# Kernel optimization log

Hardware: AMD Instinct MI355X
Metric: run time of the kernel (lower is better)

Reference implementation:

```python
import jax, jax.numpy as jnp
import numpy as np

B, DIM, H, W = 8, 384, 64, 64
HEADS, KD, RATIO = 8, 32, 2
D = RATIO * KD            # 64, per-head value dim
NH_KD = HEADS * KD        # 256
DH = HEADS * D            # 512
N = H * W


def conv1x1_bn(x, Wc, scale, bias):
    # 1x1 conv (no bias) + BatchNorm2d in eval mode folds to per-channel affine.
    y = jnp.einsum('bchw,oc->bohw', x, Wc)
    return y * scale[:, None, None] + bias[:, None, None]


def setup_inputs() -> dict:
    key = jax.random.key(0)
    ks = jax.random.split(key, 13)
    f32 = jnp.float32
    inp = {
        'x': jax.random.normal(ks[0], (B, DIM, H, W), f32),
        'Wq': jax.random.normal(ks[1], (NH_KD, DIM), f32) * (1.0 / np.sqrt(DIM)),
        'sq': jax.random.uniform(ks[2], (NH_KD,), f32, 0.5, 1.5),
        'bq': jax.random.normal(ks[3], (NH_KD,), f32) * 0.1,
        'Wk': jax.random.normal(ks[4], (NH_KD, DIM), f32) * (1.0 / np.sqrt(DIM)),
        'sk': jax.random.uniform(ks[5], (NH_KD,), f32, 0.5, 1.5),
        'bk': jax.random.normal(ks[6], (NH_KD,), f32) * 0.1,
        'Wv': jax.random.normal(ks[7], (DH, DIM), f32) * (1.0 / np.sqrt(DIM)),
        'sv': jax.random.uniform(ks[8], (DH,), f32, 0.5, 1.5),
        'bv': jax.random.normal(ks[9], (DH,), f32) * 0.1,
        'Wp': jax.random.normal(ks[10], (DIM, DH), f32) * (1.0 / np.sqrt(DH)),
        'sp': jax.random.uniform(ks[11], (DIM,), f32, 0.5, 1.5),
        'bp': jax.random.normal(ks[12], (DIM,), f32) * 0.1,
    }
    return inp


def reference(x, Wq, sq, bq, Wk, sk, bk, Wv, sv, bv, Wp, sp, bp):
    # Q/K/V projections (1x1 conv + BN), reshaped to per-head [B, h, c, N]
    q = conv1x1_bn(x, Wq, sq, bq).reshape(B, HEADS, KD, N)
    k = conv1x1_bn(x, Wk, sk, bk).reshape(B, HEADS, KD, N)
    v = conv1x1_bn(x, Wv, sv, bv).reshape(B, HEADS, D, N)
    # dual softmax: keys over spatial dim, queries over channel dim
    key_sm = jax.nn.softmax(k, axis=3)
    query_sm = jax.nn.softmax(q, axis=2)
    # context = key @ value^T : [B,h,kd,d]
    context = jnp.einsum('bhkn,bhdn->bhkd', key_sm, v)
    # attended = context^T @ query : [B,h,d,N]
    attended = jnp.einsum('bhkd,bhkn->bhdn', context, query_sm)
    attended = attended.reshape(B, DH, H, W)
    # proj: activation (ReLU) then 1x1 conv + BN
    out = conv1x1_bn(jax.nn.relu(attended), Wp, sp, bp)
    return out
```

## Files before the change

kernel.cpp:

```cpp
#include <hip/hip_runtime.h>

typedef __attribute__((ext_vector_type(8))) short bf16x8;
typedef __attribute__((ext_vector_type(4))) float f32x4;
typedef __attribute__((ext_vector_type(4))) unsigned short us4;

__device__ __forceinline__ unsigned short f2bf(float f) {
    unsigned int u = __builtin_bit_cast(unsigned int, f);
    u = (u + 0x7FFFu + ((u >> 16) & 1u)) >> 16;
    return (unsigned short)u;
}
__device__ __forceinline__ float bf2f(unsigned short h) {
    return __builtin_bit_cast(float, (unsigned int)h << 16);
}

__global__ __launch_bounds__(256) void fold_weights_k(
    const float* __restrict__ Wq, const float* __restrict__ sq, const float* __restrict__ bq,
    const float* __restrict__ Wk, const float* __restrict__ sk, const float* __restrict__ bk,
    const float* __restrict__ Wv, const float* __restrict__ sv, const float* __restrict__ bv,
    const float* __restrict__ Wp, const float* __restrict__ sp,
    unsigned short* __restrict__ WqkvP, unsigned short* __restrict__ Wpf, float* __restrict__ bqkvP)
{
    int i = blockIdx.x * 256 + threadIdx.x;
    if (i < 393216) {
        int r = i / 384, c = i - r * 384;
        int head = r >> 7, t = r & 127;
        float w, s;
        if (t < 32)      { int ch = head * 32 + t;        w = Wq[ch * 384 + c]; s = sq[ch]; }
        else if (t < 64) { int ch = head * 32 + (t - 32); w = Wk[ch * 384 + c]; s = sk[ch]; }
        else             { int ch = head * 64 + (t - 64); w = Wv[ch * 384 + c]; s = sv[ch]; }
        WqkvP[i] = f2bf(w * s);
    } else if (i < 589824) {
        int j = i - 393216;
        Wpf[j] = f2bf(Wp[j] * sp[j >> 9]);
    } else if (i < 590848) {
        int r = i - 589824;
        int head = r >> 7, t = r & 127;
        bqkvP[r] = (t < 32) ? bq[head * 32 + t]
                 : (t < 64) ? bk[head * 32 + (t - 32)]
                            : bv[head * 64 + (t - 64)];
    }
}

__global__ __launch_bounds__(256) void transpose_x_k(const float* __restrict__ x,
                                                     unsigned short* __restrict__ xT)
{
    __shared__ unsigned short t[64][72];
    const int b = blockIdx.z, cb = blockIdx.y << 6, nb = blockIdx.x << 6;
    const int tid = threadIdx.x;
    const float* xb = x + ((long)b * 384 + cb) * 4096 + nb;
    const int n4 = (tid & 15) * 4;
    #pragma unroll
    for (int p = 0; p < 4; ++p) {
        int c = (tid >> 4) + p * 16;
        float4 v = *reinterpret_cast<const float4*>(xb + (long)c * 4096 + n4);
        us4 o = { f2bf(v.x), f2bf(v.y), f2bf(v.z), f2bf(v.w) };
        *reinterpret_cast<us4*>(&t[c][n4]) = o;
    }
    __syncthreads();
    const int c4 = (tid & 15) * 4;
    unsigned short* ob = xT + ((long)b * 4096 + nb) * 384 + cb;
    #pragma unroll
    for (int p = 0; p < 4; ++p) {
        int n = (tid >> 4) + p * 16;
        us4 o = { t[c4][n], t[c4 + 1][n], t[c4 + 2][n], t[c4 + 3][n] };
        *reinterpret_cast<us4*>(ob + (long)n * 384 + c4) = o;
    }
}

__global__ __launch_bounds__(256, 3) void gemm_qkv_k(
    const unsigned short* __restrict__ A,
    const unsigned short* __restrict__ Bt,
    const float* __restrict__ bias,
    unsigned short* __restrict__ q_out,
    float* __restrict__ part,
    float* __restrict__ psums)
{
    __shared__ unsigned short As[3 * 4096];
    __shared__ unsigned short Bs[3 * 4096];
    const int tid = threadIdx.x;
    const int lane = tid & 63;
    const int w = tid >> 6, wr = w >> 1, wc = w & 1;
    const int li = lane & 15, g = lane >> 4;
    const int b = blockIdx.z, head = blockIdx.y, chunk = blockIdx.x;
    const int n0 = chunk * 128, m0 = head * 128;
    const unsigned short* Bb = Bt + (long)b * 4096 * 384;

    const int i0 = tid, i1 = tid + 256;
    const int p0 = i0 >> 3, v0 = (i0 & 7) ^ (p0 & 7);
    const int p1 = i1 >> 3, v1 = (i1 & 7) ^ (p1 & 7);
    const long ro0 = (long)(p0 * 2 + (v0 >> 2)) * 384 + (v0 & 3) * 8;
    const long ro1 = (long)(p1 * 2 + (v1 >> 2)) * 384 + (v1 & 3) * 8;
    const long aro0 = (long)m0 * 384 + ro0, aro1 = (long)m0 * 384 + ro1;
    const long bro0 = (long)n0 * 384 + ro0, bro1 = (long)n0 * 384 + ro1;

#define STAGE(kt) { const int _bf = (kt) % 3; const int _k0 = (kt) * 32; \
    __builtin_amdgcn_global_load_lds( \
        (const __attribute__((address_space(1))) void*)(A + aro0 + _k0), \
        (__attribute__((address_space(3))) void*)(As + _bf * 4096 + (size_t)i0 * 8), 16, 0, 0); \
    __builtin_amdgcn_global_load_lds( \
        (const __attribute__((address_space(1))) void*)(A + aro1 + _k0), \
        (__attribute__((address_space(3))) void*)(As + _bf * 4096 + (size_t)i1 * 8), 16, 0, 0); \
    __builtin_amdgcn_global_load_lds( \
        (const __attribute__((address_space(1))) void*)(Bb + bro0 + _k0), \
        (__attribute__((address_space(3))) void*)(Bs + _bf * 4096 + (size_t)i0 * 8), 16, 0, 0); \
    __builtin_amdgcn_global_load_lds( \
        (const __attribute__((address_space(1))) void*)(Bb + bro1 + _k0), \
        (__attribute__((address_space(3))) void*)(Bs + _bf * 4096 + (size_t)i1 * 8), 16, 0, 0); }

    STAGE(0); STAGE(1);

    f32x4 acc[4][4];
    #pragma unroll
    for (int i = 0; i < 4; ++i)
        #pragma unroll
        for (int j = 0; j < 4; ++j) acc[i][j] = (f32x4){0.f, 0.f, 0.f, 0.f};

    #pragma unroll
    for (int kt = 0; kt < 12; ++kt) {
        if (kt < 11) asm volatile("s_waitcnt vmcnt(4)\n\ts_barrier" ::: "memory");
        else         asm volatile("s_waitcnt vmcnt(0)\n\ts_barrier" ::: "memory");

        const unsigned short* Ab = As + (kt % 3) * 4096;
        const unsigned short* Bl = Bs + (kt % 3) * 4096;

        bf16x8 av[4], bv[4];
        #pragma unroll
        for (int mf = 0; mf < 4; ++mf) {
            int r = wr * 64 + mf * 16 + li;
            int p = r >> 1;
            int slot = (((r & 1) * 4 + g) ^ (p & 7));
            av[mf] = *reinterpret_cast<const bf16x8*>(Ab + p * 64 + slot * 8);
        }
        #pragma unroll
        for (int nf = 0; nf < 4; ++nf) {
            int r = wc * 64 + nf * 16 + li;
            int p = r >> 1;
            int slot = (((r & 1) * 4 + g) ^ (p & 7));
            bv[nf] = *reinterpret_cast<const bf16x8*>(Bl + p * 64 + slot * 8);
        }
        if (kt < 10) STAGE(kt + 2);
        __builtin_amdgcn_s_setprio(1);
        #pragma unroll
        for (int mf = 0; mf < 4; ++mf)
            #pragma unroll
            for (int nf = 0; nf < 4; ++nf)
                acc[mf][nf] = __builtin_amdgcn_mfma_f32_16x16x32_bf16(av[mf], bv[nf], acc[mf][nf], 0, 0, 0);
        __builtin_amdgcn_s_setprio(0);
    }
#undef STAGE

    __syncthreads();

    unsigned short* Ksh = As;
    unsigned short* Vsh = As + 4096;
    float* psl = reinterpret_cast<float*>(Bs);

    if (wr == 0) {
        #pragma unroll
        for (int mf = 0; mf < 2; ++mf) {
            int ml = mf * 16 + g * 4;
            #pragma unroll
            for (int nf = 0; nf < 4; ++nf) {
                int n = n0 + wc * 64 + nf * 16 + li;
                f32x4 v = acc[mf][nf];
                us4 o = { f2bf(v.x + bias[m0 + ml]),     f2bf(v.y + bias[m0 + ml + 1]),
                          f2bf(v.z + bias[m0 + ml + 2]), f2bf(v.w + bias[m0 + ml + 3]) };
                *reinterpret_cast<us4*>(q_out + (((long)b * 4096 + n) << 8) + head * 32 + ml) = o;
            }
        }
        float rs[2][4] = {{0.f,0.f,0.f,0.f},{0.f,0.f,0.f,0.f}};
        #pragma unroll
        for (int mm = 0; mm < 2; ++mm) {
            #pragma unroll
            for (int nf = 0; nf < 4; ++nf) {
                int nl = wc * 64 + nf * 16 + li;
                f32x4 v = acc[mm + 2][nf];
                #pragma unroll
                for (int r = 0; r < 4; ++r) {
                    int kd = mm * 16 + g * 4 + r;
                    float e = __expf(v[r] + bias[m0 + 32 + kd]);
                    rs[mm][r] += e;
                    Ksh[kd * 128 + ((((nl >> 3) ^ (kd & 7)) << 3) | (nl & 7))] = f2bf(e);
                }
            }
        }
        #pragma unroll
        for (int mm = 0; mm < 2; ++mm)
            #pragma unroll
            for (int r = 0; r < 4; ++r) {
                float s = rs[mm][r];
                s += __shfl_xor(s, 1); s += __shfl_xor(s, 2);
                s += __shfl_xor(s, 4); s += __shfl_xor(s, 8);
                if (li == 0) psl[wc * 32 + mm * 16 + g * 4 + r] = s;
            }
    } else {
        #pragma unroll
        for (int mf = 0; mf < 4; ++mf) {
            #pragma unroll
            for (int nf = 0; nf < 4; ++nf) {
                int nl = wc * 64 + nf * 16 + li;
                f32x4 v = acc[mf][nf];
                #pragma unroll
                for (int r = 0; r < 4; ++r) {
                    int d = mf * 16 + g * 4 + r;
                    Vsh[d * 128 + ((((nl >> 3) ^ (d & 7)) << 3) | (nl & 7))] =
                        f2bf(v[r] + bias[m0 + 64 + d]);
                }
            }
        }
    }
    __syncthreads();

    f32x4 c2[2] = {(f32x4){0.f,0.f,0.f,0.f}, (f32x4){0.f,0.f,0.f,0.f}};
    #pragma unroll
    for (int ks = 0; ks < 4; ++ks) {
        int rd = w * 16 + li;
        bf16x8 a0 = *reinterpret_cast<const bf16x8*>(Ksh + li * 128        + ((((ks * 4 + g) ^ (li & 7)) << 3)));
        bf16x8 a1 = *reinterpret_cast<const bf16x8*>(Ksh + (16 + li) * 128 + ((((ks * 4 + g) ^ ((16 + li) & 7)) << 3)));
        bf16x8 bb = *reinterpret_cast<const bf16x8*>(Vsh + rd * 128        + ((((ks * 4 + g) ^ (rd & 7)) << 3)));
        c2[0] = __builtin_amdgcn_mfma_f32_16x16x32_bf16(a0, bb, c2[0], 0, 0, 0);
        c2[1] = __builtin_amdgcn_mfma_f32_16x16x32_bf16(a1, bb, c2[1], 0, 0, 0);
    }
    const int bh = b * 8 + head;
    const long pbase = ((long)chunk * 64 + bh) * 2048;
    #pragma unroll
    for (int mm = 0; mm < 2; ++mm)
        #pragma unroll
        for (int r = 0; r < 4; ++r)
            part[pbase + (mm * 16 + g * 4 + r) * 64 + w * 16 + li] = c2[mm][r];
    if (tid < 32)
        psums[((long)chunk * 64 + bh) * 32 + tid] = psl[tid] + psl[32 + tid];
}

__global__ __launch_bounds__(256) void ctx_reduce_k(const float* __restrict__ part,
                                                    const float* __restrict__ psums,
                                                    unsigned short* __restrict__ ctxT)
{
    int t = blockIdx.x * 256 + threadIdx.x;
    int bh = t >> 11, i = t & 2047;
    int kd = i & 31, d = i >> 5;
    float s = 0.f, den = 0.f;
    #pragma unroll
    for (int c = 0; c < 32; ++c) {
        s   += part[((long)c * 64 + bh) * 2048 + kd * 64 + d];
        den += psums[((long)c * 64 + bh) * 32 + kd];
    }
    ctxT[t] = f2bf(s / den);
}

__global__ __launch_bounds__(512, 2) void proj_fused_k(
    const unsigned short* __restrict__ Wpf,
    const unsigned short* __restrict__ qT,
    const unsigned short* __restrict__ ctxT,
    const float* __restrict__ bp,
    float* __restrict__ out)
{
    __shared__ unsigned short Bsh[128 * 64];
    __shared__ unsigned short As[2][384 * 64];
    const int tid = threadIdx.x, lane = tid & 63, w = tid >> 6;
    const int li = lane & 15, g = lane >> 4;
    const int b = blockIdx.y, n0 = blockIdx.x * 128;

#define PROJ_STAGE(buf, s) { \
    _Pragma("unroll") \
    for (int j = 0; j < 6; ++j) { \
        int idx = j * 512 + tid; \
        int r = idx >> 3; \
        int ls = ((idx & 7) ^ (r & 7)) * 8; \
        __builtin_amdgcn_global_load_lds( \
            (const __attribute__((address_space(1))) void*)(Wpf + (long)r * 512 + (s) * 64 + ls), \
            (__attribute__((address_space(3))) void*)(As[buf] + (size_t)idx * 8), 16, 0, 0); \
    } }

    PROJ_STAGE(0, 0);

    f32x4 acc[3][8];
    #pragma unroll
    for (int i = 0; i < 3; ++i)
        #pragma unroll
        for (int j = 0; j < 8; ++j) acc[i][j] = (f32x4){0.f, 0.f, 0.f, 0.f};

    for (int s = 0; s < 8; ++s) {
        const unsigned short* cb = ctxT + ((long)b * 8 + s) * 2048;
        bf16x8 ca[4], pb;
        #pragma unroll
        for (int df = 0; df < 4; ++df)
            ca[df] = *reinterpret_cast<const bf16x8*>(cb + (df * 16 + li) * 32 + g * 8);
        {
            int n = n0 + w * 16 + li;
            bf16x8 r = *reinterpret_cast<const bf16x8*>(
                qT + (((long)b * 4096 + n) << 8) + s * 32 + g * 8);
            float f[8];
            float mx = -1e30f;
            #pragma unroll
            for (int j = 0; j < 8; ++j) { f[j] = bf2f((unsigned short)r[j]); mx = fmaxf(mx, f[j]); }
            mx = fmaxf(mx, __shfl_xor(mx, 16));
            mx = fmaxf(mx, __shfl_xor(mx, 32));
            float sm = 0.f;
            #pragma unroll
            for (int j = 0; j < 8; ++j) { f[j] = __expf(f[j] - mx); sm += f[j]; }
            sm += __shfl_xor(sm, 16);
            sm += __shfl_xor(sm, 32);
            float inv = 1.f / sm;
            #pragma unroll
            for (int j = 0; j < 8; ++j) pb[j] = (short)f2bf(f[j] * inv);
        }
        us4 bw[4];
        #pragma unroll
        for (int df = 0; df < 4; ++df) {
            f32x4 d = (f32x4){0.f, 0.f, 0.f, 0.f};
            d = __builtin_amdgcn_mfma_f32_16x16x32_bf16(ca[df], pb, d, 0, 0, 0);
            bw[df] = (us4){ f2bf(fmaxf(d.x, 0.f)), f2bf(fmaxf(d.y, 0.f)),
                            f2bf(fmaxf(d.z, 0.f)), f2bf(fmaxf(d.w, 0.f)) };
        }

        __syncthreads();

        if (s < 7) PROJ_STAGE((s + 1) & 1, s + 1);

        #pragma unroll
        for (int df = 0; df < 4; ++df) {
            int n = w * 16 + li;
            int slot = (df * 2 + (g >> 1)) ^ (n & 7);
            *reinterpret_cast<us4*>(Bsh + n * 64 + slot * 8 + (g & 1) * 4) = bw[df];
        }

        asm volatile("s_waitcnt lgkmcnt(0)\n\ts_barrier" ::: "memory");
        __builtin_amdgcn_sched_barrier(0);

        const unsigned short* Ab = As[s & 1];
        #pragma unroll
        for (int kk = 0; kk < 2; ++kk) {
            bf16x8 av[3], bv[8];
            #pragma unroll
            for (int mf = 0; mf < 3; ++mf) {
                int row = w * 48 + mf * 16 + li;
                int ps = ((kk * 4 + g) ^ (row & 7)) * 8;
                av[mf] = *reinterpret_cast<const bf16x8*>(Ab + row * 64 + ps);
            }
            #pragma unroll
            for (int nf = 0; nf < 8; ++nf) {
                int nn = nf * 16 + li;
                int ps = ((kk * 4 + g) ^ (nn & 7)) * 8;
                bv[nf] = *reinterpret_cast<const bf16x8*>(Bsh + nn * 64 + ps);
            }
            #pragma unroll
            for (int mf = 0; mf < 3; ++mf)
                #pragma unroll
                for (int nf = 0; nf < 8; ++nf)
                    acc[mf][nf] = __builtin_amdgcn_mfma_f32_16x16x32_bf16(av[mf], bv[nf], acc[mf][nf], 0, 0, 0);
        }
    }
#undef PROJ_STAGE

    #pragma unroll
    for (int mf = 0; mf < 3; ++mf) {
        int m = w * 48 + mf * 16 + g * 4;
        #pragma unroll
        for (int nf = 0; nf < 8; ++nf) {
            int n = n0 + nf * 16 + li;
            f32x4 v = acc[mf][nf];
            #pragma unroll
            for (int r = 0; r < 4; ++r)
                out[((long)b * 384 + m + r) * 4096 + n] = v[r] + bp[m + r];
        }
    }
}

extern "C" void kernel_launch(void* const* d_in, const int* in_sizes, int n_in,
                              void* d_out, int out_size, void* d_ws, size_t ws_size,
                              hipStream_t stream) {
    (void)in_sizes; (void)n_in; (void)out_size; (void)ws_size;
    const float* x  = (const float*)d_in[0];
    const float* Wq = (const float*)d_in[1];
    const float* sq = (const float*)d_in[2];
    const float* bq = (const float*)d_in[3];
    const float* Wk = (const float*)d_in[4];
    const float* sk = (const float*)d_in[5];
    const float* bk = (const float*)d_in[6];
    const float* Wv = (const float*)d_in[7];
    const float* sv = (const float*)d_in[8];
    const float* bv = (const float*)d_in[9];
    const float* Wp = (const float*)d_in[10];
    const float* sp = (const float*)d_in[11];
    const float* bp = (const float*)d_in[12];
    float* out = (float*)d_out;

    char* wsb = (char*)d_ws;
    unsigned short* Wqkv  = (unsigned short*)(wsb);
    unsigned short* Wpf   = (unsigned short*)(wsb + 786432);
    float*          bqkv  = (float*)(wsb + 1179648);
    unsigned short* ctxT  = (unsigned short*)(wsb + 1183744);
    float*          part  = (float*)(wsb + 1445888);
    float*          psums = (float*)(wsb + 18223104);
    unsigned short* xT    = (unsigned short*)(wsb + 18485248);
    unsigned short* qT    = (unsigned short*)(wsb + 43651072);

    fold_weights_k<<<2308, 256, 0, stream>>>(Wq, sq, bq, Wk, sk, bk, Wv, sv, bv, Wp, sp,
                                             Wqkv, Wpf, bqkv);
    transpose_x_k<<<dim3(64, 6, 8), 256, 0, stream>>>(x, xT);
    gemm_qkv_k<<<dim3(32, 8, 8), 256, 0, stream>>>(Wqkv, xT, bqkv, qT, part, psums);
    ctx_reduce_k<<<512, 256, 0, stream>>>(part, psums, ctxT);
    proj_fused_k<<<dim3(32, 8), 512, 0, stream>>>(Wpf, qT, ctxT, bp, out);
}
```

Measured before the change: 101.9 us.

## Fuse x transpose and bf16 conversion into QKV GEMM B-tile loading

Removes the separate transpose_x_k kernel and its bf16 xT workspace. The QKV GEMM now reads fp32 x directly into registers, converts to bf16 and writes swizzled tiles into LDS, with a register double buffer alongside the async A loads. This saves a kernel launch and a full write and read of the transposed input, at the cost of heavier per-iteration register use and an extra LDS write plus barrier in the main loop. Each block now reads x in fp32, twice the bytes of bf16, and the tile is re-read by all 8 head blocks.

New measurement: 98.50 us, median of 2. 1.03x faster.

```diff
diff --git a/kernel.cpp b/kernel.cpp
--- a/kernel.cpp
+++ b/kernel.cpp
@@ -41,35 +41,9 @@
     }
 }
 
-__global__ __launch_bounds__(256) void transpose_x_k(const float* __restrict__ x,
-                                                     unsigned short* __restrict__ xT)
-{
-    __shared__ unsigned short t[64][72];
-    const int b = blockIdx.z, cb = blockIdx.y << 6, nb = blockIdx.x << 6;
-    const int tid = threadIdx.x;
-    const float* xb = x + ((long)b * 384 + cb) * 4096 + nb;
-    const int n4 = (tid & 15) * 4;
-    #pragma unroll
-    for (int p = 0; p < 4; ++p) {
-        int c = (tid >> 4) + p * 16;
-        float4 v = *reinterpret_cast<const float4*>(xb + (long)c * 4096 + n4);
-        us4 o = { f2bf(v.x), f2bf(v.y), f2bf(v.z), f2bf(v.w) };
-        *reinterpret_cast<us4*>(&t[c][n4]) = o;
-    }
-    __syncthreads();
-    const int c4 = (tid & 15) * 4;
-    unsigned short* ob = xT + ((long)b * 4096 + nb) * 384 + cb;
-    #pragma unroll
-    for (int p = 0; p < 4; ++p) {
-        int n = (tid >> 4) + p * 16;
-        us4 o = { t[c4][n], t[c4 + 1][n], t[c4 + 2][n], t[c4 + 3][n] };
-        *reinterpret_cast<us4*>(ob + (long)n * 384 + c4) = o;
-    }
-}
-
 __global__ __launch_bounds__(256, 3) void gemm_qkv_k(
     const unsigned short* __restrict__ A,
-    const unsigned short* __restrict__ Bt,
+    const float* __restrict__ x,
     const float* __restrict__ bias,
     unsigned short* __restrict__ q_out,
     float* __restrict__ part,
@@ -83,31 +57,42 @@
     const int li = lane & 15, g = lane >> 4;
     const int b = blockIdx.z, head = blockIdx.y, chunk = blockIdx.x;
     const int n0 = chunk * 128, m0 = head * 128;
-    const unsigned short* Bb = Bt + (long)b * 4096 * 384;
+    const float* xb = x + (long)b * 384 * 4096 + n0 + 2 * lane;
 
     const int i0 = tid, i1 = tid + 256;
     const int p0 = i0 >> 3, v0 = (i0 & 7) ^ (p0 & 7);
     const int p1 = i1 >> 3, v1 = (i1 & 7) ^ (p1 & 7);
-    const long ro0 = (long)(p0 * 2 + (v0 >> 2)) * 384 + (v0 & 3) * 8;
-    const long ro1 = (long)(p1 * 2 + (v1 >> 2)) * 384 + (v1 & 3) * 8;
-    const long aro0 = (long)m0 * 384 + ro0, aro1 = (long)m0 * 384 + ro1;
-    const long bro0 = (long)n0 * 384 + ro0, bro1 = (long)n0 * 384 + ro1;
-
-#define STAGE(kt) { const int _bf = (kt) % 3; const int _k0 = (kt) * 32; \
+    const long aro0 = (long)m0 * 384 + (long)(p0 * 2 + (v0 >> 2)) * 384 + (v0 & 3) * 8;
+    const long aro1 = (long)m0 * 384 + (long)(p1 * 2 + (v1 >> 2)) * 384 + (v1 & 3) * 8;
+
+#define ISSUE_A(kt) { const int _bf = (kt) % 3; const int _k0 = (kt) * 32; \
     __builtin_amdgcn_global_load_lds( \
         (const __attribute__((address_space(1))) void*)(A + aro0 + _k0), \
         (__attribute__((address_space(3))) void*)(As + _bf * 4096 + (size_t)i0 * 8), 16, 0, 0); \
     __builtin_amdgcn_global_load_lds( \
         (const __attribute__((address_space(1))) void*)(A + aro1 + _k0), \
-        (__attribute__((address_space(3))) void*)(As + _bf * 4096 + (size_t)i1 * 8), 16, 0, 0); \
-    __builtin_amdgcn_global_load_lds( \
-        (const __attribute__((address_space(1))) void*)(Bb + bro0 + _k0), \
-        (__attribute__((address_space(3))) void*)(Bs + _bf * 4096 + (size_t)i0 * 8), 16, 0, 0); \
-    __builtin_amdgcn_global_load_lds( \
-        (const __attribute__((address_space(1))) void*)(Bb + bro1 + _k0), \
-        (__attribute__((address_space(3))) void*)(Bs + _bf * 4096 + (size_t)i1 * 8), 16, 0, 0); }
-
-    STAGE(0); STAGE(1);
+        (__attribute__((address_space(3))) void*)(As + _bf * 4096 + (size_t)i1 * 8), 16, 0, 0); }
+
+#define ISSUE_B(kt, breg) { const int _k0 = (kt) * 32 + w * 8; \
+    _Pragma("unroll") \
+    for (int j = 0; j < 8; ++j) \
+        breg[j] = *reinterpret_cast<const float2*>(xb + (long)(_k0 + j) * 4096); }
+
+#define WRITE_B(breg, _bf) { \
+    bf16x8 pk0, pk1; \
+    _Pragma("unroll") \
+    for (int j = 0; j < 8; ++j) { \
+        pk0[j] = (short)f2bf(breg[j].x); pk1[j] = (short)f2bf(breg[j].y); } \
+    int s0 = w ^ (lane & 7), s1 = (4 + w) ^ (lane & 7); \
+    *reinterpret_cast<bf16x8*>(Bs + (_bf) * 4096 + lane * 64 + s0 * 8) = pk0; \
+    *reinterpret_cast<bf16x8*>(Bs + (_bf) * 4096 + lane * 64 + s1 * 8) = pk1; }
+
+    float2 bregA[8], bregB[8];
+    ISSUE_A(0); ISSUE_B(0, bregA);
+    ISSUE_A(1); ISSUE_B(1, bregB);
+    WRITE_B(bregA, 0);
+    asm volatile("s_waitcnt vmcnt(10) lgkmcnt(0)\n\ts_barrier" ::: "memory");
+    __builtin_amdgcn_sched_barrier(0);
 
     f32x4 acc[4][4];
     #pragma unroll
@@ -117,9 +102,6 @@
 
     #pragma unroll
     for (int kt = 0; kt < 12; ++kt) {
-        if (kt < 11) asm volatile("s_waitcnt vmcnt(4)\n\ts_barrier" ::: "memory");
-        else         asm volatile("s_waitcnt vmcnt(0)\n\ts_barrier" ::: "memory");
-
         const unsigned short* Ab = As + (kt % 3) * 4096;
         const unsigned short* Bl = Bs + (kt % 3) * 4096;
 
@@ -138,7 +120,11 @@
             int slot = (((r & 1) * 4 + g) ^ (p & 7));
             bv[nf] = *reinterpret_cast<const bf16x8*>(Bl + p * 64 + slot * 8);
         }
-        if (kt < 10) STAGE(kt + 2);
+        if (kt < 10) {
+            ISSUE_A(kt + 2);
+            if (kt & 1) { ISSUE_B(kt + 2, bregB) }
+            else        { ISSUE_B(kt + 2, bregA) }
+        }
         __builtin_amdgcn_s_setprio(1);
         #pragma unroll
         for (int mf = 0; mf < 4; ++mf)
@@ -146,8 +132,16 @@
             for (int nf = 0; nf < 4; ++nf)
                 acc[mf][nf] = __builtin_amdgcn_mfma_f32_16x16x32_bf16(av[mf], bv[nf], acc[mf][nf], 0, 0, 0);
         __builtin_amdgcn_s_setprio(0);
-    }
-#undef STAGE
+        if (kt < 11) {
+            if (kt & 1) { WRITE_B(bregA, (kt + 1) % 3) }
+            else        { WRITE_B(bregB, (kt + 1) % 3) }
+            asm volatile("s_waitcnt lgkmcnt(0)\n\ts_barrier" ::: "memory");
+            __builtin_amdgcn_sched_barrier(0);
+        }
+    }
+#undef ISSUE_A
+#undef ISSUE_B
+#undef WRITE_B
 
     __syncthreads();
 
@@ -393,13 +387,11 @@
     unsigned short* ctxT  = (unsigned short*)(wsb + 1183744);
     float*          part  = (float*)(wsb + 1445888);
     float*          psums = (float*)(wsb + 18223104);
-    unsigned short* xT    = (unsigned short*)(wsb + 18485248);
-    unsigned short* qT    = (unsigned short*)(wsb + 43651072);
+    unsigned short* qT    = (unsigned short*)(wsb + 18485248);
 
     fold_weights_k<<<2308, 256, 0, stream>>>(Wq, sq, bq, Wk, sk, bk, Wv, sv, bv, Wp, sp,
                                              Wqkv, Wpf, bqkv);
-    transpose_x_k<<<dim3(64, 6, 8), 256, 0, stream>>>(x, xT);
-    gemm_qkv_k<<<dim3(32, 8, 8), 256, 0, stream>>>(Wqkv, xT, bqkv, qT, part, psums);
+    gemm_qkv_k<<<dim3(32, 8, 8), 256, 0, stream>>>(Wqkv, x, bqkv, qT, part, psums);
     ctx_reduce_k<<<512, 256, 0, stream>>>(part, psums, ctxT);
     proj_fused_k<<<dim3(32, 8), 512, 0, stream>>>(Wpf, qT, ctxT, bp, out);
 }
```
